# Optimization experiments

Measured on AMD Instinct MI355X. Metric: run time of the kernel, lower is better.

Reference implementation:

```python
import jax, jax.numpy as jnp
import numpy as np

B = 8          # number of point clouds
N = 1024       # points per cloud
RATIO = 0.125  # fps sampling ratio -> S = 128 centers per cloud
K = 32         # neighborhood size
EMB = 384      # embedding size


def _mlp(x, Wa, ba, Wb, bb):
    # Linear -> ReLU -> Linear (torch_geometric-style MLP, no act on last layer)
    return jax.nn.relu(x @ Wa + ba) @ Wb + bb


def _fps_single(p, n_samples):
    # iterative farthest point sampling on one cloud p: [N,3]; deterministic start idx 0
    n = p.shape[0]
    def step(carry, _):
        mind, last = carry
        d = jnp.sum((p - p[last]) ** 2, axis=-1)      # [N]
        mind = jnp.minimum(mind, d)
        nxt = jnp.argmax(mind).astype(jnp.int32)
        return (mind, nxt), last
    init = (jnp.full((n,), jnp.inf, p.dtype), jnp.array(0, jnp.int32))
    _, idx = jax.lax.scan(step, init, None, length=n_samples)
    return idx  # [n_samples]


def setup_inputs() -> dict:
    key = jax.random.key(0)
    ks = jax.random.split(key, 9)
    def lin(k, fan_in, fan_out):
        bound = 1.0 / np.sqrt(fan_in)
        kw, kb = jax.random.split(k)
        W = jax.random.uniform(kw, (fan_in, fan_out), jnp.float32, -bound, bound)
        b = jax.random.uniform(kb, (fan_out,), jnp.float32, -bound, bound)
        return W, b
    W1a, b1a = lin(ks[0], 3, 128)
    W1b, b1b = lin(ks[1], 128, 256)
    W2a, b2a = lin(ks[2], 512, 512)
    W2b, b2b = lin(ks[3], 512, EMB)
    pos = jax.random.normal(ks[4], (B * N, 3), jnp.float32)
    batch = jnp.repeat(jnp.arange(B, dtype=jnp.int32), N)
    return {"pos": pos, "batch": batch,
            "W1a": W1a, "b1a": b1a, "W1b": W1b, "b1b": b1b,
            "W2a": W2a, "b2a": b2a, "W2b": W2b, "b2b": b2b}


def reference(pos, batch, W1a, b1a, W1b, b1b, W2a, b2a, W2b, b2b):
    # batch is contiguous with N points per cloud -> reshape to [B,N,3]
    pos3 = pos.reshape(B, N, 3)
    S = int(N * RATIO)

    # --- FPS per cloud ---
    idx = jax.vmap(lambda p: _fps_single(p, S))(pos3)              # [B,S]
    seeds = jnp.take_along_axis(pos3, idx[..., None], axis=1)       # [B,S,3]

    # --- kNN: for each seed, K nearest points within its cloud ---
    d = jnp.sum((seeds[:, :, None, :] - pos3[:, None, :, :]) ** 2, axis=-1)  # [B,S,N]
    _, nbr = jax.lax.top_k(-d, K)                                   # [B,S,K]

    # --- PointConv: gather -> mlp1 -> max -> concat -> mlp2 -> max ---
    nbr_pos = jax.vmap(lambda p, i: p[i])(pos3, nbr)                # [B,S,K,3]
    rel = nbr_pos - seeds[:, :, None, :]                            # pos_j - pos_i
    f = _mlp(rel, W1a, b1a, W1b, b1b)                               # [B,S,K,256]
    g = jnp.max(f, axis=2)                                          # [B,S,256]
    h = jnp.concatenate(
        [jnp.broadcast_to(g[:, :, None, :], f.shape), f], axis=-1)  # [B,S,K,512]
    e = _mlp(h, W2a, b2a, W2b, b2b)                                 # [B,S,K,EMB]
    out = jnp.max(e, axis=2)                                        # [B,S,EMB]
    return out.reshape(B * S, EMB)
```

## Files before the change

kernel.cpp:

```cpp
#include <hip/hip_runtime.h>
#include <math.h>

#define BB   8
#define NN   1024
#define SS   128
#define KK   32
#define EMB  384

#define KP1  136
#define KP2  264
#define KP3  520

typedef __attribute__((ext_vector_type(4))) float f32x4;
typedef __attribute__((ext_vector_type(8))) _Float16 f16x8;

__device__ __forceinline__ f32x4 mfma16h(f16x8 a, f16x8 b, f32x4 c) {
    return __builtin_amdgcn_mfma_f32_16x16x32_f16(a, b, c, 0, 0, 0);
}
__device__ __forceinline__ f32x4 vmax4(f32x4 a, f32x4 b) {
    f32x4 r;
    r.x = fmaxf(a.x, b.x); r.y = fmaxf(a.y, b.y);
    r.z = fmaxf(a.z, b.z); r.w = fmaxf(a.w, b.w);
    return r;
}

__global__ __launch_bounds__(256, 1) void pre_kernel(
    const float* __restrict__ pos, float* __restrict__ seed_pos,
    const float* __restrict__ W1b, const float* __restrict__ W2a,
    const float* __restrict__ W2b,
    _Float16* __restrict__ W1bt, _Float16* __restrict__ W2at,
    _Float16* __restrict__ W2bt)
{
    __shared__ float s_cloud[3][NN];
    __shared__ __align__(16) float s_red[64];
    __shared__ float tile[32][33];
    const int bid = blockIdx.x;
    if (bid < BB) {
        const int b = bid;
        const float* p = pos + (size_t)b * NN * 3;
        for (int k = 0; k < 4; ++k) {
            const int i = threadIdx.x + k * 256;
            s_cloud[0][i] = p[i * 3 + 0];
            s_cloud[1][i] = p[i * 3 + 1];
            s_cloud[2][i] = p[i * 3 + 2];
        }
        __syncthreads();
        if (threadIdx.x >= 64) return;
        const int l = threadIdx.x;

        float px[16], py[16], pz[16], mind[16];
#pragma unroll
        for (int r = 0; r < 16; ++r) {
            const int i = l * 16 + r;
            px[r] = p[i * 3 + 0];
            py[r] = p[i * 3 + 1];
            pz[r] = p[i * 3 + 2];
            mind[r] = INFINITY;
        }
#pragma unroll
        for (int r = 0; r < 16; ++r) {
            asm volatile("" : "+v"(px[r]), "+v"(py[r]), "+v"(pz[r]));
        }

        int gi = 0;
        for (int s = 0; s < SS; ++s) {
            const float sxv = s_cloud[0][gi];
            const float syv = s_cloud[1][gi];
            const float szv = s_cloud[2][gi];
            if (l == 0) {
                seed_pos[((size_t)b * SS + s) * 3 + 0] = sxv;
                seed_pos[((size_t)b * SS + s) * 3 + 1] = syv;
                seed_pos[((size_t)b * SS + s) * 3 + 2] = szv;
            }
            if (s == SS - 1) break;
#pragma unroll
            for (int r = 0; r < 16; ++r) {
                const float dx = __fsub_rn(px[r], sxv);
                const float dy = __fsub_rn(py[r], syv);
                const float dz = __fsub_rn(pz[r], szv);
                const float d = __fadd_rn(__fadd_rn(__fmul_rn(dx, dx), __fmul_rn(dy, dy)),
                                          __fmul_rn(dz, dz));
                mind[r] = fminf(mind[r], d);
            }
            float t8[8];
#pragma unroll
            for (int r = 0; r < 8; ++r) t8[r] = fmaxf(mind[r], mind[r + 8]);
            const float q0 = fmaxf(fmaxf(t8[0], t8[1]), fmaxf(t8[2], t8[3]));
            const float q1 = fmaxf(fmaxf(t8[4], t8[5]), fmaxf(t8[6], t8[7]));
            const float lm = fmaxf(q0, q1);

            s_red[l] = lm;
            const f32x4* rp = (const f32x4*)s_red;
            const f32x4 u0 = vmax4(vmax4(rp[0],  rp[1]),  vmax4(rp[2],  rp[3]));
            const f32x4 u1 = vmax4(vmax4(rp[4],  rp[5]),  vmax4(rp[6],  rp[7]));
            const f32x4 u2 = vmax4(vmax4(rp[8],  rp[9]),  vmax4(rp[10], rp[11]));
            const f32x4 u3 = vmax4(vmax4(rp[12], rp[13]), vmax4(rp[14], rp[15]));
            const f32x4 uu = vmax4(vmax4(u0, u1), vmax4(u2, u3));
            const float gmax = fmaxf(fmaxf(uu.x, uu.y), fmaxf(uu.z, uu.w));

            int bl = 16;
#pragma unroll
            for (int r = 15; r >= 0; --r) {
                bl = (mind[r] == gmax) ? r : bl;
            }
            const unsigned long long mball = __ballot(bl != 16);
            const int ln = (int)__ffsll((unsigned long long)mball) - 1;
            gi = __builtin_amdgcn_readlane(l * 16 + bl, ln);
        }
        return;
    }

    int tid = bid - BB;
    const float* src;
    _Float16* dh;
    int N, Kp, koff, kt, nt;
    if (tid < 32) {
        src = W1b; dh = W1bt; N = 256; Kp = KP1; koff = 0;
        kt = tid >> 3; nt = tid & 7;
    } else if (tid < 160) {
        tid -= 32;
        src = W2a; dh = W2at; N = 512; Kp = KP2; koff = 256;
        kt = tid >> 4; nt = tid & 15;
    } else {
        tid -= 160;
        src = W2b; dh = W2bt; N = 384; Kp = KP3; koff = 0;
        kt = tid / 12; nt = tid % 12;
    }
    const int k0 = kt * 32, n0 = nt * 32;
    const int tx = threadIdx.x & 31, ty = threadIdx.x >> 5;
#pragma unroll
    for (int i = 0; i < 4; ++i) {
        const int kl = ty + i * 8;
        tile[kl][tx] = src[(size_t)(k0 + kl + koff) * N + n0 + tx];
    }
    __syncthreads();
#pragma unroll
    for (int i = 0; i < 4; ++i) {
        const int nl = ty + i * 8;
        dh[(size_t)(n0 + nl) * Kp + k0 + tx] = (_Float16)tile[tx][nl];
    }
}

__global__ __launch_bounds__(512) void knn_kernel(
    const float* __restrict__ pos,
    const float* __restrict__ seed_pos,
    int* __restrict__ nbr)
{
    __shared__ float sx_[NN], sy_[NN], sz_[NN];
    const int blk = blockIdx.x;
    const int b   = blk >> 4;
    const int t   = threadIdx.x;
    const int w   = t >> 6;
    const int l   = t & 63;
    const float* p = pos + (size_t)b * NN * 3;

    for (int i = t; i < NN; i += 512) {
        sx_[i] = p[i * 3 + 0];
        sy_[i] = p[i * 3 + 1];
        sz_[i] = p[i * 3 + 2];
    }
    __syncthreads();

    const int gsid = b * SS + (blk & 15) * 8 + w;
    const float cx = seed_pos[gsid * 3 + 0];
    const float cy = seed_pos[gsid * 3 + 1];
    const float cz = seed_pos[gsid * 3 + 2];

    float d[16];
#pragma unroll
    for (int r = 0; r < 16; ++r) {
        const int i = r * 64 + l;
        const float dx = __fsub_rn(sx_[i], cx);
        const float dy = __fsub_rn(sy_[i], cy);
        const float dz = __fsub_rn(sz_[i], cz);
        d[r] = __fadd_rn(__fadd_rn(__fmul_rn(dx, dx), __fmul_rn(dy, dy)),
                         __fmul_rn(dz, dz));
    }

    for (int it = 0; it < KK; ++it) {
        float best = INFINITY;
        int bi = NN;
#pragma unroll
        for (int r = 0; r < 16; ++r) {
            if (d[r] < best) { best = d[r]; bi = r * 64 + l; }
        }
#pragma unroll
        for (int off = 1; off < 64; off <<= 1) {
            const float ov = __shfl_xor(best, off);
            const int   oi = __shfl_xor(bi, off);
            if (ov < best || (ov == best && oi < bi)) { best = ov; bi = oi; }
        }
        const int wr = bi >> 6, wl = bi & 63;
#pragma unroll
        for (int r = 0; r < 16; ++r) {
            if (r == wr && l == wl) d[r] = INFINITY;
        }
        if (l == 0) nbr[(size_t)gsid * KK + it] = bi;
    }
}

__global__ __launch_bounds__(1024) void conv_kernel(
    const float* __restrict__ pos,
    const float* __restrict__ seed_pos,
    const int* __restrict__ nbr,
    const float* __restrict__ W1a, const float* __restrict__ b1a,
    const float* __restrict__ b1b,
    const float* __restrict__ W2a, const float* __restrict__ b2a,
    const float* __restrict__ b2b,
    const _Float16* __restrict__ W1bt, const _Float16* __restrict__ W2at,
    const _Float16* __restrict__ W2bt,
    float* __restrict__ out)
{
    __shared__ __align__(16) unsigned char smem[144896];
    unsigned char* sBig = smem;
    float* s_g    = (float*)(smem + 131072);
    float* s_base = (float*)(smem + 135168);
    float* s_rel  = (float*)(smem + 143360);

    const int blk = blockIdx.x;
    const int t   = threadIdx.x;
    const int w   = t >> 6;
    const int l   = t & 63;
    const int lg  = l >> 4;
    const int l15 = l & 15;

    if (t < 128) {
        const int sl   = t >> 5;
        const int gsid = blk * 4 + sl;
        const int b    = gsid >> 7;
        const int pi   = nbr[(size_t)gsid * KK + (t & 31)];
        const float* pp = pos + ((size_t)b * NN + pi) * 3;
        s_rel[t * 3 + 0] = pp[0] - seed_pos[gsid * 3 + 0];
        s_rel[t * 3 + 1] = pp[1] - seed_pos[gsid * 3 + 1];
        s_rel[t * 3 + 2] = pp[2] - seed_pos[gsid * 3 + 2];
    }
    __syncthreads();

    {
        const int j  = t & 127;
        const int rg = t >> 7;
        const float w0 = W1a[j], w1 = W1a[128 + j], w2 = W1a[256 + j], bb = b1a[j];
#pragma unroll
        for (int rr = 0; rr < 16; ++rr) {
            const int row = rg * 16 + rr;
            float v = fmaf(s_rel[row * 3 + 2], w2,
                      fmaf(s_rel[row * 3 + 1], w1,
                      fmaf(s_rel[row * 3 + 0], w0, bb)));
            v = fmaxf(v, 0.0f);
            const int byte = (j * 2) ^ ((row & 7) << 4);
            *(_Float16*)(sBig + row * 256 + byte) = (_Float16)v;
        }
    }
    __syncthreads();

    f32x4 C1[8];
#pragma unroll
    for (int m = 0; m < 8; ++m) C1[m] = (f32x4){0.f, 0.f, 0.f, 0.f};
#pragma unroll
    for (int ks = 0; ks < 4; ++ks) {
        const int ncol = w * 16 + l15;
        const f16x8 bh = *(const f16x8*)(W1bt + (size_t)ncol * KP1 + lg * 8 + ks * 32);
#pragma unroll
        for (int m = 0; m < 8; ++m) {
            const int row = m * 16 + l15;
            const int byte = (lg * 16 + ks * 64) ^ ((row & 7) << 4);
            const f16x8 ah = *(const f16x8*)(sBig + row * 256 + byte);
            C1[m] = mfma16h(ah, bh, C1[m]);
        }
    }
    {
        const int col = w * 16 + l15;
        const float bias = b1b[col];
        float pm0 = -INFINITY, pm1 = -INFINITY, pm2 = -INFINITY, pm3 = -INFINITY;
#pragma unroll
        for (int m = 0; m < 8; ++m)
#pragma unroll
            for (int r = 0; r < 4; ++r) {
                const float v = C1[m][r] + bias;
                if (m < 2)      pm0 = fmaxf(pm0, v);
                else if (m < 4) pm1 = fmaxf(pm1, v);
                else if (m < 6) pm2 = fmaxf(pm2, v);
                else            pm3 = fmaxf(pm3, v);
            }
        pm0 = fmaxf(pm0, __shfl_xor(pm0, 16)); pm0 = fmaxf(pm0, __shfl_xor(pm0, 32));
        pm1 = fmaxf(pm1, __shfl_xor(pm1, 16)); pm1 = fmaxf(pm1, __shfl_xor(pm1, 32));
        pm2 = fmaxf(pm2, __shfl_xor(pm2, 16)); pm2 = fmaxf(pm2, __shfl_xor(pm2, 32));
        pm3 = fmaxf(pm3, __shfl_xor(pm3, 16)); pm3 = fmaxf(pm3, __shfl_xor(pm3, 32));
        if (lg == 0) {
            s_g[0 * 256 + col] = pm0;
            s_g[1 * 256 + col] = pm1;
            s_g[2 * 256 + col] = pm2;
            s_g[3 * 256 + col] = pm3;
        }
    }
    __syncthreads();

    {
        const int col = w * 16 + l15;
        const float bias = b1b[col];
#pragma unroll
        for (int m = 0; m < 8; ++m)
#pragma unroll
            for (int r = 0; r < 4; ++r) {
                const float v = C1[m][r] + bias;
                const int row = m * 16 + lg * 4 + r;
                const int byte = (col * 2) ^ ((row & 7) << 4);
                *(_Float16*)(sBig + row * 512 + byte) = (_Float16)v;
            }
    }

    {
        const int col = t & 511;
        const int sp  = t >> 9;
        float a0 = b2a[col], a1 = b2a[col];
        const float* g0 = s_g + (sp * 2) * 256;
        const float* g1 = s_g + (sp * 2 + 1) * 256;
#pragma unroll 4
        for (int jj = 0; jj < 256; ++jj) {
            const float w_ = W2a[(size_t)jj * 512 + col];
            a0 = fmaf(g0[jj], w_, a0);
            a1 = fmaf(g1[jj], w_, a1);
        }
        s_base[(sp * 2) * 512 + col]     = a0;
        s_base[(sp * 2 + 1) * 512 + col] = a1;
    }
    __syncthreads();

    f32x4 C2[8][2];
#pragma unroll
    for (int m = 0; m < 8; ++m)
#pragma unroll
        for (int n = 0; n < 2; ++n) C2[m][n] = (f32x4){0.f, 0.f, 0.f, 0.f};
#pragma unroll 2
    for (int ks = 0; ks < 8; ++ks) {
        f16x8 bh[2];
#pragma unroll
        for (int n = 0; n < 2; ++n) {
            const int ncol = w * 32 + n * 16 + l15;
            bh[n] = *(const f16x8*)(W2at + (size_t)ncol * KP2 + lg * 8 + ks * 32);
        }
#pragma unroll
        for (int m = 0; m < 8; ++m) {
            const int row = m * 16 + l15;
            const int byte = (lg * 16 + ks * 64) ^ ((row & 7) << 4);
            const f16x8 ah = *(const f16x8*)(sBig + row * 512 + byte);
            C2[m][0] = mfma16h(ah, bh[0], C2[m][0]);
            C2[m][1] = mfma16h(ah, bh[1], C2[m][1]);
        }
    }
    __syncthreads();

#pragma unroll
    for (int n = 0; n < 2; ++n) {
        const int col = w * 32 + n * 16 + l15;
#pragma unroll
        for (int m = 0; m < 8; ++m) {
            const float bs = s_base[(m >> 1) * 512 + col];
#pragma unroll
            for (int r = 0; r < 4; ++r) {
                const float v = fmaxf(C2[m][n][r] + bs, 0.0f);
                const int row = m * 16 + lg * 4 + r;
                const int byte = (col * 2) ^ ((row & 7) << 4);
                *(_Float16*)(sBig + row * 1024 + byte) = (_Float16)v;
            }
        }
    }
    __syncthreads();

    if (w < 12) {
        f32x4 C3[8][2];
#pragma unroll
        for (int m = 0; m < 8; ++m)
#pragma unroll
            for (int n = 0; n < 2; ++n) C3[m][n] = (f32x4){0.f, 0.f, 0.f, 0.f};
#pragma unroll 2
        for (int ks = 0; ks < 16; ++ks) {
            f16x8 bh[2];
#pragma unroll
            for (int n = 0; n < 2; ++n) {
                const int ncol = w * 32 + n * 16 + l15;
                bh[n] = *(const f16x8*)(W2bt + (size_t)ncol * KP3 + lg * 8 + ks * 32);
            }
#pragma unroll
            for (int m = 0; m < 8; ++m) {
                const int row = m * 16 + l15;
                const int byte = (lg * 16 + ks * 64) ^ ((row & 7) << 4);
                const f16x8 ah = *(const f16x8*)(sBig + row * 1024 + byte);
                C3[m][0] = mfma16h(ah, bh[0], C3[m][0]);
                C3[m][1] = mfma16h(ah, bh[1], C3[m][1]);
            }
        }
#pragma unroll
        for (int n = 0; n < 2; ++n) {
            const int col = w * 32 + n * 16 + l15;
            float pm0 = -INFINITY, pm1 = -INFINITY, pm2 = -INFINITY, pm3 = -INFINITY;
#pragma unroll
            for (int m = 0; m < 8; ++m)
#pragma unroll
                for (int r = 0; r < 4; ++r) {
                    const float v = C3[m][n][r];
                    if (m < 2)      pm0 = fmaxf(pm0, v);
                    else if (m < 4) pm1 = fmaxf(pm1, v);
                    else if (m < 6) pm2 = fmaxf(pm2, v);
                    else            pm3 = fmaxf(pm3, v);
                }
            pm0 = fmaxf(pm0, __shfl_xor(pm0, 16)); pm0 = fmaxf(pm0, __shfl_xor(pm0, 32));
            pm1 = fmaxf(pm1, __shfl_xor(pm1, 16)); pm1 = fmaxf(pm1, __shfl_xor(pm1, 32));
            pm2 = fmaxf(pm2, __shfl_xor(pm2, 16)); pm2 = fmaxf(pm2, __shfl_xor(pm2, 32));
            pm3 = fmaxf(pm3, __shfl_xor(pm3, 16)); pm3 = fmaxf(pm3, __shfl_xor(pm3, 32));
            if (lg == 0) {
                const float bb = b2b[col];
                out[(size_t)(blk * 4 + 0) * EMB + col] = pm0 + bb;
                out[(size_t)(blk * 4 + 1) * EMB + col] = pm1 + bb;
                out[(size_t)(blk * 4 + 2) * EMB + col] = pm2 + bb;
                out[(size_t)(blk * 4 + 3) * EMB + col] = pm3 + bb;
            }
        }
    }
}

extern "C" void kernel_launch(void* const* d_in, const int* in_sizes, int n_in,
                              void* d_out, int out_size, void* d_ws, size_t ws_size,
                              hipStream_t stream)
{
    const float* pos = (const float*)d_in[0];
    const float* W1a = (const float*)d_in[2];
    const float* b1a = (const float*)d_in[3];
    const float* W1b = (const float*)d_in[4];
    const float* b1b = (const float*)d_in[5];
    const float* W2a = (const float*)d_in[6];
    const float* b2a = (const float*)d_in[7];
    const float* W2b = (const float*)d_in[8];
    const float* b2b = (const float*)d_in[9];
    float* out = (float*)d_out;

    unsigned char* ws = (unsigned char*)d_ws;
    float* seed_pos = (float*)(ws + 0);
    int*   nbr      = (int*)(ws + 16384);
    _Float16* W1bt  = (_Float16*)(ws + 147456);
    _Float16* W2at  = (_Float16*)(ws + 217088);
    _Float16* W2bt  = (_Float16*)(ws + 487424);

    pre_kernel<<<BB + 352, 256, 0, stream>>>(pos, seed_pos, W1b, W2a, W2b,
                                             W1bt, W2at, W2bt);
    knn_kernel<<<BB * SS / 8, 512, 0, stream>>>(pos, seed_pos, nbr);
    conv_kernel<<<BB * SS / 4, 1024, 0, stream>>>(pos, seed_pos, nbr,
                                                  W1a, b1a, b1b, W2a, b2a, b2b,
                                                  W1bt, W2at, W2bt, out);
}
```

Before: 180.3 us.

## Rewrite FPS as 256-thread block with shared-memory tree argmax reduction

```diff
diff --git a/kernel.cpp b/kernel.cpp
--- a/kernel.cpp
+++ b/kernel.cpp
@@ -17,95 +17,71 @@
 __device__ __forceinline__ f32x4 mfma16h(f16x8 a, f16x8 b, f32x4 c) {
     return __builtin_amdgcn_mfma_f32_16x16x32_f16(a, b, c, 0, 0, 0);
 }
-__device__ __forceinline__ f32x4 vmax4(f32x4 a, f32x4 b) {
-    f32x4 r;
-    r.x = fmaxf(a.x, b.x); r.y = fmaxf(a.y, b.y);
-    r.z = fmaxf(a.z, b.z); r.w = fmaxf(a.w, b.w);
-    return r;
-}
-
-__global__ __launch_bounds__(256, 1) void pre_kernel(
+
+__global__ __launch_bounds__(256) void pre_kernel(
     const float* __restrict__ pos, float* __restrict__ seed_pos,
     const float* __restrict__ W1b, const float* __restrict__ W2a,
     const float* __restrict__ W2b,
     _Float16* __restrict__ W1bt, _Float16* __restrict__ W2at,
     _Float16* __restrict__ W2bt)
 {
-    __shared__ float s_cloud[3][NN];
-    __shared__ __align__(16) float s_red[64];
+    __shared__ float s_val[256];
+    __shared__ int   s_idx[256];
     __shared__ float tile[32][33];
     const int bid = blockIdx.x;
     if (bid < BB) {
         const int b = bid;
+        const int t = threadIdx.x;
         const float* p = pos + (size_t)b * NN * 3;
-        for (int k = 0; k < 4; ++k) {
-            const int i = threadIdx.x + k * 256;
-            s_cloud[0][i] = p[i * 3 + 0];
-            s_cloud[1][i] = p[i * 3 + 1];
-            s_cloud[2][i] = p[i * 3 + 2];
-        }
-        __syncthreads();
-        if (threadIdx.x >= 64) return;
-        const int l = threadIdx.x;
-
-        float px[16], py[16], pz[16], mind[16];
-#pragma unroll
-        for (int r = 0; r < 16; ++r) {
-            const int i = l * 16 + r;
+
+        float px[4], py[4], pz[4], mind[4];
+#pragma unroll
+        for (int r = 0; r < 4; ++r) {
+            const int i = t + r * 256;
             px[r] = p[i * 3 + 0];
             py[r] = p[i * 3 + 1];
             pz[r] = p[i * 3 + 2];
             mind[r] = INFINITY;
         }
-#pragma unroll
-        for (int r = 0; r < 16; ++r) {
-            asm volatile("" : "+v"(px[r]), "+v"(py[r]), "+v"(pz[r]));
-        }
-
-        int gi = 0;
+
+        int last = 0;
         for (int s = 0; s < SS; ++s) {
-            const float sxv = s_cloud[0][gi];
-            const float syv = s_cloud[1][gi];
-            const float szv = s_cloud[2][gi];
-            if (l == 0) {
-                seed_pos[((size_t)b * SS + s) * 3 + 0] = sxv;
-                seed_pos[((size_t)b * SS + s) * 3 + 1] = syv;
-                seed_pos[((size_t)b * SS + s) * 3 + 2] = szv;
+            const float sx = p[last * 3 + 0];
+            const float sy = p[last * 3 + 1];
+            const float sz = p[last * 3 + 2];
+            if (t == 0) {
+                seed_pos[((size_t)b * SS + s) * 3 + 0] = sx;
+                seed_pos[((size_t)b * SS + s) * 3 + 1] = sy;
+                seed_pos[((size_t)b * SS + s) * 3 + 2] = sz;
             }
             if (s == SS - 1) break;
-#pragma unroll
-            for (int r = 0; r < 16; ++r) {
-                const float dx = __fsub_rn(px[r], sxv);
-                const float dy = __fsub_rn(py[r], syv);
-                const float dz = __fsub_rn(pz[r], szv);
+            float best = -INFINITY;
+            int bi = 0;
+#pragma unroll
+            for (int r = 0; r < 4; ++r) {
+                const float dx = __fsub_rn(px[r], sx);
+                const float dy = __fsub_rn(py[r], sy);
+                const float dz = __fsub_rn(pz[r], sz);
                 const float d = __fadd_rn(__fadd_rn(__fmul_rn(dx, dx), __fmul_rn(dy, dy)),
                                           __fmul_rn(dz, dz));
                 mind[r] = fminf(mind[r], d);
-            }
-            float t8[8];
-#pragma unroll
-            for (int r = 0; r < 8; ++r) t8[r] = fmaxf(mind[r], mind[r + 8]);
-            const float q0 = fmaxf(fmaxf(t8[0], t8[1]), fmaxf(t8[2], t8[3]));
-            const float q1 = fmaxf(fmaxf(t8[4], t8[5]), fmaxf(t8[6], t8[7]));
-            const float lm = fmaxf(q0, q1);
-
-            s_red[l] = lm;
-            const f32x4* rp = (const f32x4*)s_red;
-            const f32x4 u0 = vmax4(vmax4(rp[0],  rp[1]),  vmax4(rp[2],  rp[3]));
-            const f32x4 u1 = vmax4(vmax4(rp[4],  rp[5]),  vmax4(rp[6],  rp[7]));
-            const f32x4 u2 = vmax4(vmax4(rp[8],  rp[9]),  vmax4(rp[10], rp[11]));
-            const f32x4 u3 = vmax4(vmax4(rp[12], rp[13]), vmax4(rp[14], rp[15]));
-            const f32x4 uu = vmax4(vmax4(u0, u1), vmax4(u2, u3));
-            const float gmax = fmaxf(fmaxf(uu.x, uu.y), fmaxf(uu.z, uu.w));
-
-            int bl = 16;
-#pragma unroll
-            for (int r = 15; r >= 0; --r) {
-                bl = (mind[r] == gmax) ? r : bl;
-            }
-            const unsigned long long mball = __ballot(bl != 16);
-            const int ln = (int)__ffsll((unsigned long long)mball) - 1;
-            gi = __builtin_amdgcn_readlane(l * 16 + bl, ln);
+                if (mind[r] > best) { best = mind[r]; bi = t + r * 256; }
+            }
+            s_val[t] = best;
+            s_idx[t] = bi;
+            __syncthreads();
+            for (int off = 128; off > 0; off >>= 1) {
+                if (t < off) {
+                    const float v2 = s_val[t + off];
+                    const int   i2 = s_idx[t + off];
+                    if (v2 > s_val[t] || (v2 == s_val[t] && i2 < s_idx[t])) {
+                        s_val[t] = v2; s_idx[t] = i2;
+                    }
+                }
+                __syncthreads();
+            }
+            last = s_idx[0];
+            __syncthreads();
         }
         return;
     }
```

Result: slower. 225.1 us (+24.8%).
